# Performance work log

Hardware: AMD Instinct MI355X
Metric: run time of the kernel (lower is better)

Reference implementation:

```python
import jax, jax.numpy as jnp
import numpy as np

EPS = 1e-5

def _bn(h, g, b, m, v):
    # inference-mode batchnorm, channel axis = 1
    shape = (1, -1) + (1,) * (h.ndim - 2)
    scale = g.reshape(shape) / jnp.sqrt(v.reshape(shape) + EPS)
    return (h - m.reshape(shape)) * scale + b.reshape(shape)

def setup_inputs() -> dict:
    B, Cin, Cout, N, K = 2, 64, 64, 50000, 16
    key = jax.random.key(0)
    ks = jax.random.split(key, 24)
    def bn_params(i, C):
        g = 1.0 + 0.1 * jax.random.normal(ks[i], (C,), jnp.float32)
        b = 0.1 * jax.random.normal(ks[i + 1], (C,), jnp.float32)
        m = 0.1 * jax.random.normal(ks[i + 2], (C,), jnp.float32)
        v = jax.random.uniform(ks[i + 3], (C,), jnp.float32, 0.5, 1.5)
        return g, b, m, v
    bn0_g, bn0_b, bn0_m, bn0_v = bn_params(0, Cin)
    bn2a_g, bn2a_b, bn2a_m, bn2a_v = bn_params(4, Cin)
    bn2b_g, bn2b_b, bn2b_m, bn2b_v = bn_params(8, Cout)
    x = jax.random.normal(ks[12], (B, Cin, N), jnp.float32)
    neighbors = jax.random.randint(ks[13], (B, K, N), 0, N, jnp.int32)
    w1 = 0.05 * jax.random.normal(ks[14], (Cout, Cin), jnp.float32)
    b1 = 0.05 * jax.random.normal(ks[15], (Cout,), jnp.float32)
    w2a = 0.05 * jax.random.normal(ks[16], (Cout, Cin), jnp.float32)
    w2b = 0.05 * jax.random.normal(ks[17], (Cout, Cout), jnp.float32)
    wf = 0.05 * jax.random.normal(ks[18], (Cout, 2 * Cout), jnp.float32)
    bf = 0.05 * jax.random.normal(ks[19], (Cout,), jnp.float32)
    return {"x": x, "neighbors": neighbors,
            "bn0_g": bn0_g, "bn0_b": bn0_b, "bn0_m": bn0_m, "bn0_v": bn0_v,
            "w1": w1, "b1": b1,
            "bn2a_g": bn2a_g, "bn2a_b": bn2a_b, "bn2a_m": bn2a_m, "bn2a_v": bn2a_v,
            "w2a": w2a,
            "bn2b_g": bn2b_g, "bn2b_b": bn2b_b, "bn2b_m": bn2b_m, "bn2b_v": bn2b_v,
            "w2b": w2b, "wf": wf, "bf": bf}

def reference(x, neighbors, bn0_g, bn0_b, bn0_m, bn0_v, w1, b1,
              bn2a_g, bn2a_b, bn2a_m, bn2a_v, w2a,
              bn2b_g, bn2b_b, bn2b_m, bn2b_v, w2b, wf, bf):
    # x: (B, Cin, N), neighbors: (B, K, N) int indices into N
    xn = _bn(x, bn0_g, bn0_b, bn0_m, bn0_v)                    # BatchNorm1d
    point = jnp.einsum('oc,bcn->bon', w1, xn) + b1[None, :, None]  # conv1 (1x1)
    idx = neighbors[:, 1:, :]                                   # (B, K-1, N); skip self (col 0)
    # gathered[b,c,k,n] = xn[b,c, idx[b,k,n]]
    gathered = jax.vmap(lambda xb, ib: xb[:, ib])(xn, idx)      # (B, C, K-1, N)
    diff = jnp.transpose(gathered, (0, 1, 3, 2)) - xn[:, :, :, None]  # (B, C, N, K-1)
    h = _bn(diff, bn2a_g, bn2a_b, bn2a_m, bn2a_v)               # BatchNorm2d
    h = jnp.einsum('oc,bcnk->bonk', w2a, h)                     # Conv2d 1x1, no bias
    h = jax.nn.relu(_bn(h, bn2b_g, bn2b_b, bn2b_m, bn2b_v))
    h = jnp.einsum('oc,bcnk->bonk', w2b, h)                     # Conv2d 1x1, no bias
    neigh = h.max(axis=-1)                                      # max over K-1 neighbors
    cat = jnp.concatenate([point, neigh], axis=1)               # (B, 2*Cout, N)
    return jnp.einsum('oc,bcn->bon', wf, cat) + bf[None, :, None]
```

## Files before the change

### kernel.cpp

```cpp
#include <hip/hip_runtime.h>
#include <hip/hip_bf16.h>

typedef __bf16 bf16x8 __attribute__((ext_vector_type(8)));
typedef float f32x4 __attribute__((ext_vector_type(4)));
typedef unsigned int uint32x4 __attribute__((ext_vector_type(4)));

#define NPT 50000

#define OFF_Y    0u
#define OFF_PRM  12800000u
#define OFF_W2   12801024u
#define OFF_WP   12809216u
#define OFF_W2B  12817408u
#define OFF_WN   12825600u
#define OFF_FLAG 12833792u

__global__ __launch_bounds__(256) void precompute_kernel(
    const void* bn0_g, const void* bn0_b, const void* bn0_m, const void* bn0_v,
    const void* w1, const void* b1,
    const void* bn2a_g, const void* bn2a_b, const void* bn2a_m, const void* bn2a_v,
    const void* w2a,
    const void* bn2b_g, const void* bn2b_b, const void* bn2b_m, const void* bn2b_v,
    const void* w2b, const void* wf, const void* bfv,
    float* __restrict__ prm, __bf16* __restrict__ W2bf, __bf16* __restrict__ Wpbf,
    __bf16* __restrict__ W2Bbf, __bf16* __restrict__ Wnbf, int* __restrict__ flagp)
{
    __shared__ __bf16 w1s[4096];
    __shared__ __bf16 wfs[8192];
    __shared__ __bf16 w2as[4096];
    __shared__ float b1s[64], bfs[64], s2a[64], t2a[64], s2b[64], t2b[64];
    __shared__ int sflag;
    int t = threadIdx.x;

    if (t == 0) {
        const unsigned short* u = (const unsigned short*)bn0_v;
        int cnt = 0;
        for (int i = 0; i < 64; ++i) {
            float f = __uint_as_float(((unsigned int)u[i]) << 16);
            if (f > 0.4f && f < 1.6f) cnt++;
        }
        int fv = (cnt >= 60) ? 1 : 0;
        sflag = fv;
        *flagp = fv;
    }
    __syncthreads();
    int fl = sflag;

    if (fl) {
        const __bf16* W1  = (const __bf16*)w1;
        const __bf16* W2A = (const __bf16*)w2a;
        const __bf16* WF  = (const __bf16*)wf;
        const __bf16* W2B = (const __bf16*)w2b;
        for (int i = t; i < 4096; i += 256) { w1s[i] = W1[i]; w2as[i] = W2A[i]; W2Bbf[i] = W2B[i]; }
        for (int i = t; i < 8192; i += 256) wfs[i] = WF[i];
        if (t < 64) {
            float s0 = (float)((const __bf16*)bn0_g)[t] / sqrtf((float)((const __bf16*)bn0_v)[t] + 1e-5f);
            prm[t] = s0;
            prm[64 + t] = (float)((const __bf16*)bn0_b)[t] - (float)((const __bf16*)bn0_m)[t] * s0;
            float sa = (float)((const __bf16*)bn2a_g)[t] / sqrtf((float)((const __bf16*)bn2a_v)[t] + 1e-5f);
            s2a[t] = sa;
            t2a[t] = (float)((const __bf16*)bn2a_b)[t] - (float)((const __bf16*)bn2a_m)[t] * sa;
            float sb = (float)((const __bf16*)bn2b_g)[t] / sqrtf((float)((const __bf16*)bn2b_v)[t] + 1e-5f);
            s2b[t] = sb;
            t2b[t] = (float)((const __bf16*)bn2b_b)[t] - (float)((const __bf16*)bn2b_m)[t] * sb;
            b1s[t] = (float)((const __bf16*)b1)[t];
            bfs[t] = (float)((const __bf16*)bfv)[t];
        }
    } else {
        const float* W1  = (const float*)w1;
        const float* W2A = (const float*)w2a;
        const float* WF  = (const float*)wf;
        const float* W2B = (const float*)w2b;
        for (int i = t; i < 4096; i += 256) { w1s[i] = (__bf16)W1[i]; w2as[i] = (__bf16)W2A[i]; W2Bbf[i] = (__bf16)W2B[i]; }
        for (int i = t; i < 8192; i += 256) wfs[i] = (__bf16)WF[i];
        if (t < 64) {
            float s0 = ((const float*)bn0_g)[t] / sqrtf(((const float*)bn0_v)[t] + 1e-5f);
            prm[t] = s0;
            prm[64 + t] = ((const float*)bn0_b)[t] - ((const float*)bn0_m)[t] * s0;
            float sa = ((const float*)bn2a_g)[t] / sqrtf(((const float*)bn2a_v)[t] + 1e-5f);
            s2a[t] = sa;
            t2a[t] = ((const float*)bn2a_b)[t] - ((const float*)bn2a_m)[t] * sa;
            float sb = ((const float*)bn2b_g)[t] / sqrtf(((const float*)bn2b_v)[t] + 1e-5f);
            s2b[t] = sb;
            t2b[t] = ((const float*)bn2b_b)[t] - ((const float*)bn2b_m)[t] * sb;
            b1s[t] = ((const float*)b1)[t];
            bfs[t] = ((const float*)bfv)[t];
        }
    }
    __syncthreads();

    for (int e = t; e < 4096; e += 256) {
        int o = e >> 6, c = e & 63;
        W2bf[e] = (__bf16)((float)w2as[e] * s2a[c] * s2b[o]);
        Wnbf[e] = wfs[o * 128 + 64 + c];
        float acc = 0.f;
        for (int m = 0; m < 64; ++m)
            acc += (float)wfs[o * 128 + m] * (float)w1s[m * 64 + c];
        Wpbf[e] = (__bf16)acc;
    }
    if (t < 64) {
        float acc = 0.f, accb = 0.f;
        for (int c = 0; c < 64; ++c) {
            acc  += (float)w2as[t * 64 + c] * t2a[c];
            accb += (float)wfs[t * 128 + c] * b1s[c];
        }
        prm[128 + t] = s2b[t] * acc + t2b[t];
        prm[192 + t] = accb + bfs[t];
    }
}

__global__ __launch_bounds__(256) void pass1_kernel(
    const void* x, const float* __restrict__ prm,
    const __bf16* __restrict__ W2bf, __bf16* __restrict__ Y,
    const int* __restrict__ flagp)
{
    __shared__ float xs[64][65];
    int bid = blockIdx.x;
    int b = bid / 782;
    int n0 = (bid % 782) * 64;
    int npts = NPT - n0; if (npts > 64) npts = 64;
    int fl = *flagp;

    if (npts == 64) {
        if (fl) {
            const __bf16* xb = (const __bf16*)x + (size_t)b * 64 * NPT + n0;
            for (int i = threadIdx.x; i < 512; i += 256) {
                int c = i >> 3, q = (i & 7) * 8;
                bf16x8 v = *(const bf16x8*)(xb + (size_t)c * NPT + q);
                #pragma unroll
                for (int e = 0; e < 8; ++e)
                    xs[q + e][c] = fmaf((float)v[e], prm[c], prm[64 + c]);
            }
        } else {
            const float* xb = (const float*)x + (size_t)b * 64 * NPT + n0;
            for (int i = threadIdx.x; i < 1024; i += 256) {
                int c = i >> 4, q = (i & 15) * 4;
                float4 v = *(const float4*)(xb + (size_t)c * NPT + q);
                xs[q + 0][c] = fmaf(v.x, prm[c], prm[64 + c]);
                xs[q + 1][c] = fmaf(v.y, prm[c], prm[64 + c]);
                xs[q + 2][c] = fmaf(v.z, prm[c], prm[64 + c]);
                xs[q + 3][c] = fmaf(v.w, prm[c], prm[64 + c]);
            }
        }
    } else {
        if (fl) {
            const __bf16* xb = (const __bf16*)x + (size_t)b * 64 * NPT;
            for (int i = threadIdx.x; i < 4096; i += 256) {
                int c = i >> 6, p = i & 63;
                float v = (p < npts) ? (float)xb[(size_t)c * NPT + n0 + p] : 0.f;
                xs[p][c] = fmaf(v, prm[c], prm[64 + c]);
            }
        } else {
            const float* xb = (const float*)x + (size_t)b * 64 * NPT;
            for (int i = threadIdx.x; i < 4096; i += 256) {
                int c = i >> 6, p = i & 63;
                float v = (p < npts) ? xb[(size_t)c * NPT + n0 + p] : 0.f;
                xs[p][c] = fmaf(v, prm[c], prm[64 + c]);
            }
        }
    }
    __syncthreads();

    int wid = threadIdx.x >> 6, lane = threadIdx.x & 63;
    int pl = (wid << 4) + (lane & 15);
    int hq = lane >> 4;
    int c0 = hq << 3;

    bf16x8 a0, a1;
    #pragma unroll
    for (int i = 0; i < 8; ++i) {
        a0[i] = (__bf16)xs[pl][c0 + i];
        a1[i] = (__bf16)xs[pl][c0 + 32 + i];
    }

    int ob = lane & 15;
    f32x4 accY[4];
    #pragma unroll
    for (int nt = 0; nt < 4; ++nt) {
        bf16x8 w20 = *(const bf16x8*)(W2bf + (ob + 16 * nt) * 64 + c0);
        bf16x8 w21 = *(const bf16x8*)(W2bf + (ob + 16 * nt) * 64 + c0 + 32);
        f32x4 z = {0.f, 0.f, 0.f, 0.f};
        accY[nt] = __builtin_amdgcn_mfma_f32_16x16x32_bf16(a0, w20, z, 0, 0, 0);
        accY[nt] = __builtin_amdgcn_mfma_f32_16x16x32_bf16(a1, w21, accY[nt], 0, 0, 0);
    }

    #pragma unroll
    for (int nt = 0; nt < 4; ++nt) {
        #pragma unroll
        for (int i = 0; i < 4; ++i) {
            int prow = (wid << 4) + (hq << 2) + i;
            if (prow < npts)
                Y[((size_t)b * NPT + n0 + prow) * 64 + ob + 16 * nt] = (__bf16)accY[nt][i];
        }
    }
}

__global__ __launch_bounds__(256, 2) void pass2_kernel(
    const int* __restrict__ nbr, const __bf16* __restrict__ Y,
    const void* x, const float* __restrict__ prm,
    const __bf16* __restrict__ W2Bbf, const __bf16* __restrict__ Wnbf,
    const __bf16* __restrict__ Wpbf, void* out, const int* __restrict__ flagp)
{
    __shared__ float ns[2][2][16][69];
    int wid = threadIdx.x >> 6, lane = threadIdx.x & 63;
    int tile = wid >> 1, h = wid & 1;
    int gtile = blockIdx.x * 2 + tile;
    int b = gtile / 3125;
    int n0 = (gtile % 3125) << 4;
    int fl = *flagp;

    int mo = lane & 15;
    int hq = lane >> 4;
    int c0 = hq << 3;
    int nglob = n0 + mo;

    const int* nb_base = nbr + (size_t)b * 16 * NPT + NPT + nglob;
    int kbase = h * 7;
    unsigned int ju[8];
    #pragma unroll
    for (int kk = 0; kk < 8; ++kk) {
        unsigned long long a = (unsigned long long)(nb_base + (size_t)(kbase + kk) * NPT);
        asm volatile("global_load_dword %0, %1, off" : "=v"(ju[kk]) : "v"(a) : "memory");
    }
    unsigned int xr[16];
    if (fl) {
        const __bf16* xp = (const __bf16*)x + (size_t)b * 64 * NPT + nglob;
        #pragma unroll
        for (int i = 0; i < 16; ++i) {
            int c = c0 + (i >> 3) * 32 + (i & 7);
            unsigned long long a = (unsigned long long)(xp + (size_t)c * NPT);
            asm volatile("global_load_ushort %0, %1, off" : "=v"(xr[i]) : "v"(a) : "memory");
        }
    } else {
        const float* xp = (const float*)x + (size_t)b * 64 * NPT + nglob;
        #pragma unroll
        for (int i = 0; i < 16; ++i) {
            int c = c0 + (i >> 3) * 32 + (i & 7);
            unsigned long long a = (unsigned long long)(xp + (size_t)c * NPT);
            asm volatile("global_load_dword %0, %1, off" : "=v"(xr[i]) : "v"(a) : "memory");
        }
    }

    const __bf16* yrow = Y + ((size_t)b * NPT + nglob) * 64;
    bf16x8 yn0 = *(const bf16x8*)(yrow + c0);
    bf16x8 yn1 = *(const bf16x8*)(yrow + c0 + 32);
    bf16x8 wA[4][2];
    #pragma unroll
    for (int mt = 0; mt < 4; ++mt) {
        wA[mt][0] = *(const bf16x8*)(W2Bbf + (mo + 16 * mt) * 64 + c0);
        wA[mt][1] = *(const bf16x8*)(W2Bbf + (mo + 16 * mt) * 64 + c0 + 32);
    }

    asm volatile("s_waitcnt vmcnt(0)" ::: "memory");
    __builtin_amdgcn_sched_barrier(0);

    uint32x4 g0[8], g1[8];
    const char* ybase = (const char*)Y + (size_t)b * NPT * 128 + hq * 16;
    #pragma unroll
    for (int kk = 0; kk < 8; ++kk) {
        unsigned long long a0 = (unsigned long long)(ybase + (size_t)ju[kk] * 128);
        asm volatile("global_load_dwordx4 %0, %1, off" : "=v"(g0[kk]) : "v"(a0) : "memory");
        asm volatile("global_load_dwordx4 %0, %1, off offset:64" : "=v"(g1[kk]) : "v"(a0) : "memory");
    }

    float mv0[8], mv1[8];
    #pragma unroll
    for (int i = 0; i < 8; ++i) {
        mv0[i] = prm[128 + c0 + i]      - (float)yn0[i];
        mv1[i] = prm[128 + c0 + 32 + i] - (float)yn1[i];
    }

    f32x4 vmax[4];
    #pragma unroll
    for (int mt = 0; mt < 4; ++mt) vmax[mt] = {-3.0e38f, -3.0e38f, -3.0e38f, -3.0e38f};

    asm volatile("s_waitcnt vmcnt(0)" ::: "memory");
    __builtin_amdgcn_sched_barrier(0);

    #pragma unroll
    for (int kk = 0; kk < 8; ++kk) {
        bf16x8 y0 = __builtin_bit_cast(bf16x8, g0[kk]);
        bf16x8 y1 = __builtin_bit_cast(bf16x8, g1[kk]);
        bf16x8 t0, t1;
        #pragma unroll
        for (int i = 0; i < 8; ++i) {
            t0[i] = (__bf16)fmaxf((float)y0[i] + mv0[i], 0.f);
            t1[i] = (__bf16)fmaxf((float)y1[i] + mv1[i], 0.f);
        }
        #pragma unroll
        for (int mt = 0; mt < 4; ++mt) {
            f32x4 hh = {0.f, 0.f, 0.f, 0.f};
            hh = __builtin_amdgcn_mfma_f32_16x16x32_bf16(wA[mt][0], t0, hh, 0, 0, 0);
            hh = __builtin_amdgcn_mfma_f32_16x16x32_bf16(wA[mt][1], t1, hh, 0, 0, 0);
            #pragma unroll
            for (int i = 0; i < 4; ++i) vmax[mt][i] = fmaxf(vmax[mt][i], hh[i]);
        }
    }

    #pragma unroll
    for (int mt = 0; mt < 4; ++mt)
        #pragma unroll
        for (int i = 0; i < 4; ++i)
            ns[tile][h][mo][16 * mt + (hq << 2) + i] = vmax[mt][i];

    __syncthreads();

    bf16x8 nb2[2];
    #pragma unroll
    for (int ks = 0; ks < 2; ++ks)
        #pragma unroll
        for (int i = 0; i < 8; ++i) {
            int c = c0 + 32 * ks + i;
            nb2[ks][i] = (__bf16)fmaxf(ns[tile][0][mo][c], ns[tile][1][mo][c]);
        }

    bf16x8 xnb[2];
    #pragma unroll
    for (int i = 0; i < 16; ++i) {
        int c = c0 + (i >> 3) * 32 + (i & 7);
        float v = fl ? __uint_as_float(xr[i] << 16) : __uint_as_float(xr[i]);
        xnb[i >> 3][i & 7] = (__bf16)fmaf(v, prm[c], prm[64 + c]);
    }

    #pragma unroll
    for (int q = 0; q < 2; ++q) {
        int mt = 2 * h + q;
        bf16x8 wn0 = *(const bf16x8*)(Wnbf + (mo + 16 * mt) * 64 + c0);
        bf16x8 wn1 = *(const bf16x8*)(Wnbf + (mo + 16 * mt) * 64 + c0 + 32);
        bf16x8 wp0 = *(const bf16x8*)(Wpbf + (mo + 16 * mt) * 64 + c0);
        bf16x8 wp1 = *(const bf16x8*)(Wpbf + (mo + 16 * mt) * 64 + c0 + 32);
        f32x4 acc = *(const f32x4*)(prm + 192 + 16 * mt + 4 * hq);
        acc = __builtin_amdgcn_mfma_f32_16x16x32_bf16(wp0, xnb[0], acc, 0, 0, 0);
        acc = __builtin_amdgcn_mfma_f32_16x16x32_bf16(wp1, xnb[1], acc, 0, 0, 0);
        acc = __builtin_amdgcn_mfma_f32_16x16x32_bf16(wn0, nb2[0], acc, 0, 0, 0);
        acc = __builtin_amdgcn_mfma_f32_16x16x32_bf16(wn1, nb2[1], acc, 0, 0, 0);

        if (fl) {
            __bf16* ob = (__bf16*)out + (size_t)b * 64 * NPT + nglob;
            #pragma unroll
            for (int i = 0; i < 4; ++i)
                ob[(size_t)(16 * mt + (hq << 2) + i) * NPT] = (__bf16)acc[i];
        } else {
            float* ob = (float*)out + (size_t)b * 64 * NPT + nglob;
            #pragma unroll
            for (int i = 0; i < 4; ++i)
                ob[(size_t)(16 * mt + (hq << 2) + i) * NPT] = acc[i];
        }
    }
}

extern "C" void kernel_launch(void* const* d_in, const int* in_sizes, int n_in,
                              void* d_out, int out_size, void* d_ws, size_t ws_size,
                              hipStream_t stream) {
    const void* x      = d_in[0];
    const int*  nbr    = (const int*)d_in[1];

    char* ws = (char*)d_ws;
    __bf16* Y     = (__bf16*)(ws + OFF_Y);
    float*  prm   = (float*)(ws + OFF_PRM);
    __bf16* W2bf  = (__bf16*)(ws + OFF_W2);
    __bf16* Wpbf  = (__bf16*)(ws + OFF_WP);
    __bf16* W2Bbf = (__bf16*)(ws + OFF_W2B);
    __bf16* Wnbf  = (__bf16*)(ws + OFF_WN);
    int*    flagp = (int*)(ws + OFF_FLAG);

    precompute_kernel<<<1, 256, 0, stream>>>(
        d_in[2], d_in[3], d_in[4], d_in[5], d_in[6], d_in[7],
        d_in[8], d_in[9], d_in[10], d_in[11], d_in[12],
        d_in[13], d_in[14], d_in[15], d_in[16], d_in[17], d_in[18], d_in[19],
        prm, W2bf, Wpbf, W2Bbf, Wnbf, flagp);

    pass1_kernel<<<1564, 256, 0, stream>>>(x, prm, W2bf, Y, flagp);

    pass2_kernel<<<3125, 256, 0, stream>>>(nbr, Y, x, prm, W2Bbf, Wnbf, Wpbf, d_out, flagp);
}
```

Baseline: 203.6 us.

## Split pass2 neighbor work across four waves and parallelize the Wp precompute

The pass2 kernel now assigns one 16-point tile per block, with four waves each handling four neighbors instead of two waves handling eight. Partial maxima are combined through shared memory, and only two waves then load x and run the final projection. Launch bounds rise to four blocks per SM, aiming for more in-flight gathers and lower register pressure. The folded wf·w1 product is also spread over 16 extra precompute blocks instead of being computed serially in one block. The trade-offs are that half the waves sit idle during the epilogue and the x loads no longer overlap with the gathers.

```diff
diff --git a/kernel.cpp b/kernel.cpp
--- a/kernel.cpp
+++ b/kernel.cpp
@@ -14,6 +14,16 @@
 #define OFF_W2B  12817408u
 #define OFF_WN   12825600u
 #define OFF_FLAG 12833792u
+
+__device__ __forceinline__ int detect_bf16(const void* bn0_v) {
+    const unsigned short* u = (const unsigned short*)bn0_v;
+    int cnt = 0;
+    for (int i = 0; i < 64; ++i) {
+        float f = __uint_as_float(((unsigned int)u[i]) << 16);
+        if (f > 0.4f && f < 1.6f) cnt++;
+    }
+    return (cnt >= 60) ? 1 : 0;
+}
 
 __global__ __launch_bounds__(256) void precompute_kernel(
     const void* bn0_g, const void* bn0_b, const void* bn0_m, const void* bn0_v,
@@ -25,33 +35,53 @@
     float* __restrict__ prm, __bf16* __restrict__ W2bf, __bf16* __restrict__ Wpbf,
     __bf16* __restrict__ W2Bbf, __bf16* __restrict__ Wnbf, int* __restrict__ flagp)
 {
-    __shared__ __bf16 w1s[4096];
+    __shared__ int sflag;
+    int t = threadIdx.x;
+    if (t == 0) sflag = detect_bf16(bn0_v);
+    __syncthreads();
+    int fl = sflag;
+
+    if (blockIdx.x < 16) {
+        __shared__ __bf16 w1s[4096];
+        __shared__ float wfr[4][64];
+        int ob = blockIdx.x * 4;
+        if (fl) {
+            const __bf16* W1 = (const __bf16*)w1;
+            const __bf16* WF = (const __bf16*)wf;
+            for (int i = t; i < 4096; i += 256) w1s[i] = W1[i];
+            if (t < 256) {
+                int o = t >> 6, m = t & 63;
+                wfr[o][m] = (float)WF[(ob + o) * 128 + m];
+            }
+        } else {
+            const float* W1 = (const float*)w1;
+            const float* WF = (const float*)wf;
+            for (int i = t; i < 4096; i += 256) w1s[i] = (__bf16)W1[i];
+            if (t < 256) {
+                int o = t >> 6, m = t & 63;
+                wfr[o][m] = WF[(ob + o) * 128 + m];
+            }
+        }
+        __syncthreads();
+        int o = t >> 6, c = t & 63;
+        float acc = 0.f;
+        for (int m = 0; m < 64; ++m)
+            acc += wfr[o][m] * (float)w1s[m * 64 + c];
+        Wpbf[(ob + o) * 64 + c] = (__bf16)acc;
+        return;
+    }
+
     __shared__ __bf16 wfs[8192];
     __shared__ __bf16 w2as[4096];
     __shared__ float b1s[64], bfs[64], s2a[64], t2a[64], s2b[64], t2b[64];
-    __shared__ int sflag;
-    int t = threadIdx.x;
-
-    if (t == 0) {
-        const unsigned short* u = (const unsigned short*)bn0_v;
-        int cnt = 0;
-        for (int i = 0; i < 64; ++i) {
-            float f = __uint_as_float(((unsigned int)u[i]) << 16);
-            if (f > 0.4f && f < 1.6f) cnt++;
-        }
-        int fv = (cnt >= 60) ? 1 : 0;
-        sflag = fv;
-        *flagp = fv;
-    }
-    __syncthreads();
-    int fl = sflag;
+
+    if (t == 0) *flagp = fl;
 
     if (fl) {
-        const __bf16* W1  = (const __bf16*)w1;
         const __bf16* W2A = (const __bf16*)w2a;
         const __bf16* WF  = (const __bf16*)wf;
         const __bf16* W2B = (const __bf16*)w2b;
-        for (int i = t; i < 4096; i += 256) { w1s[i] = W1[i]; w2as[i] = W2A[i]; W2Bbf[i] = W2B[i]; }
+        for (int i = t; i < 4096; i += 256) { w2as[i] = W2A[i]; W2Bbf[i] = W2B[i]; }
         for (int i = t; i < 8192; i += 256) wfs[i] = WF[i];
         if (t < 64) {
             float s0 = (float)((const __bf16*)bn0_g)[t] / sqrtf((float)((const __bf16*)bn0_v)[t] + 1e-5f);
@@ -67,11 +97,10 @@
             bfs[t] = (float)((const __bf16*)bfv)[t];
         }
     } else {
-        const float* W1  = (const float*)w1;
         const float* W2A = (const float*)w2a;
         const float* WF  = (const float*)wf;
         const float* W2B = (const float*)w2b;
-        for (int i = t; i < 4096; i += 256) { w1s[i] = (__bf16)W1[i]; w2as[i] = (__bf16)W2A[i]; W2Bbf[i] = (__bf16)W2B[i]; }
+        for (int i = t; i < 4096; i += 256) { w2as[i] = (__bf16)W2A[i]; W2Bbf[i] = (__bf16)W2B[i]; }
         for (int i = t; i < 8192; i += 256) wfs[i] = (__bf16)WF[i];
         if (t < 64) {
             float s0 = ((const float*)bn0_g)[t] / sqrtf(((const float*)bn0_v)[t] + 1e-5f);
@@ -93,10 +122,6 @@
         int o = e >> 6, c = e & 63;
         W2bf[e] = (__bf16)((float)w2as[e] * s2a[c] * s2b[o]);
         Wnbf[e] = wfs[o * 128 + 64 + c];
-        float acc = 0.f;
-        for (int m = 0; m < 64; ++m)
-            acc += (float)wfs[o * 128 + m] * (float)w1s[m * 64 + c];
-        Wpbf[e] = (__bf16)acc;
     }
     if (t < 64) {
         float acc = 0.f, accb = 0.f;
@@ -195,16 +220,15 @@
     }
 }
 
-__global__ __launch_bounds__(256, 2) void pass2_kernel(
+__global__ __launch_bounds__(256, 4) void pass2_kernel(
     const int* __restrict__ nbr, const __bf16* __restrict__ Y,
     const void* x, const float* __restrict__ prm,
     const __bf16* __restrict__ W2Bbf, const __bf16* __restrict__ Wnbf,
     const __bf16* __restrict__ Wpbf, void* out, const int* __restrict__ flagp)
 {
-    __shared__ float ns[2][2][16][69];
-    int wid = threadIdx.x >> 6, lane = threadIdx.x & 63;
-    int tile = wid >> 1, h = wid & 1;
-    int gtile = blockIdx.x * 2 + tile;
+    __shared__ float ns[4][16][69];
+    int h = threadIdx.x >> 6, lane = threadIdx.x & 63;
+    int gtile = blockIdx.x;
     int b = gtile / 3125;
     int n0 = (gtile % 3125) << 4;
     int fl = *flagp;
@@ -214,31 +238,13 @@
     int c0 = hq << 3;
     int nglob = n0 + mo;
 
-    const int* nb_base = nbr + (size_t)b * 16 * NPT + NPT + nglob;
-    int kbase = h * 7;
-    unsigned int ju[8];
-    #pragma unroll
-    for (int kk = 0; kk < 8; ++kk) {
-        unsigned long long a = (unsigned long long)(nb_base + (size_t)(kbase + kk) * NPT);
+    const int* nb_base = nbr + (size_t)b * 16 * NPT + nglob;
+    unsigned int ju[4];
+    #pragma unroll
+    for (int kk = 0; kk < 4; ++kk) {
+        int kv = 4 * h + kk + 1; if (kv > 15) kv = 15;
+        unsigned long long a = (unsigned long long)(nb_base + (size_t)kv * NPT);
         asm volatile("global_load_dword %0, %1, off" : "=v"(ju[kk]) : "v"(a) : "memory");
-    }
-    unsigned int xr[16];
-    if (fl) {
-        const __bf16* xp = (const __bf16*)x + (size_t)b * 64 * NPT + nglob;
-        #pragma unroll
-        for (int i = 0; i < 16; ++i) {
-            int c = c0 + (i >> 3) * 32 + (i & 7);
-            unsigned long long a = (unsigned long long)(xp + (size_t)c * NPT);
-            asm volatile("global_load_ushort %0, %1, off" : "=v"(xr[i]) : "v"(a) : "memory");
-        }
-    } else {
-        const float* xp = (const float*)x + (size_t)b * 64 * NPT + nglob;
-        #pragma unroll
-        for (int i = 0; i < 16; ++i) {
-            int c = c0 + (i >> 3) * 32 + (i & 7);
-            unsigned long long a = (unsigned long long)(xp + (size_t)c * NPT);
-            asm volatile("global_load_dword %0, %1, off" : "=v"(xr[i]) : "v"(a) : "memory");
-        }
     }
 
     const __bf16* yrow = Y + ((size_t)b * NPT + nglob) * 64;
@@ -254,10 +260,10 @@
     asm volatile("s_waitcnt vmcnt(0)" ::: "memory");
     __builtin_amdgcn_sched_barrier(0);
 
-    uint32x4 g0[8], g1[8];
+    uint32x4 g0[4], g1[4];
     const char* ybase = (const char*)Y + (size_t)b * NPT * 128 + hq * 16;
     #pragma unroll
-    for (int kk = 0; kk < 8; ++kk) {
+    for (int kk = 0; kk < 4; ++kk) {
         unsigned long long a0 = (unsigned long long)(ybase + (size_t)ju[kk] * 128);
         asm volatile("global_load_dwordx4 %0, %1, off" : "=v"(g0[kk]) : "v"(a0) : "memory");
         asm volatile("global_load_dwordx4 %0, %1, off offset:64" : "=v"(g1[kk]) : "v"(a0) : "memory");
@@ -278,7 +284,7 @@
     __builtin_amdgcn_sched_barrier(0);
 
     #pragma unroll
-    for (int kk = 0; kk < 8; ++kk) {
+    for (int kk = 0; kk < 4; ++kk) {
         bf16x8 y0 = __builtin_bit_cast(bf16x8, g0[kk]);
         bf16x8 y1 = __builtin_bit_cast(bf16x8, g1[kk]);
         bf16x8 t0, t1;
@@ -301,50 +307,69 @@
     for (int mt = 0; mt < 4; ++mt)
         #pragma unroll
         for (int i = 0; i < 4; ++i)
-            ns[tile][h][mo][16 * mt + (hq << 2) + i] = vmax[mt][i];
+            ns[h][mo][16 * mt + (hq << 2) + i] = vmax[mt][i];
 
     __syncthreads();
 
-    bf16x8 nb2[2];
-    #pragma unroll
-    for (int ks = 0; ks < 2; ++ks)
-        #pragma unroll
-        for (int i = 0; i < 8; ++i) {
-            int c = c0 + 32 * ks + i;
-            nb2[ks][i] = (__bf16)fmaxf(ns[tile][0][mo][c], ns[tile][1][mo][c]);
-        }
-
-    bf16x8 xnb[2];
-    #pragma unroll
-    for (int i = 0; i < 16; ++i) {
-        int c = c0 + (i >> 3) * 32 + (i & 7);
-        float v = fl ? __uint_as_float(xr[i] << 16) : __uint_as_float(xr[i]);
-        xnb[i >> 3][i & 7] = (__bf16)fmaf(v, prm[c], prm[64 + c]);
-    }
-
-    #pragma unroll
-    for (int q = 0; q < 2; ++q) {
-        int mt = 2 * h + q;
-        bf16x8 wn0 = *(const bf16x8*)(Wnbf + (mo + 16 * mt) * 64 + c0);
-        bf16x8 wn1 = *(const bf16x8*)(Wnbf + (mo + 16 * mt) * 64 + c0 + 32);
-        bf16x8 wp0 = *(const bf16x8*)(Wpbf + (mo + 16 * mt) * 64 + c0);
-        bf16x8 wp1 = *(const bf16x8*)(Wpbf + (mo + 16 * mt) * 64 + c0 + 32);
-        f32x4 acc = *(const f32x4*)(prm + 192 + 16 * mt + 4 * hq);
-        acc = __builtin_amdgcn_mfma_f32_16x16x32_bf16(wp0, xnb[0], acc, 0, 0, 0);
-        acc = __builtin_amdgcn_mfma_f32_16x16x32_bf16(wp1, xnb[1], acc, 0, 0, 0);
-        acc = __builtin_amdgcn_mfma_f32_16x16x32_bf16(wn0, nb2[0], acc, 0, 0, 0);
-        acc = __builtin_amdgcn_mfma_f32_16x16x32_bf16(wn1, nb2[1], acc, 0, 0, 0);
-
+    if (h < 2) {
+        bf16x8 nb2[2];
+        #pragma unroll
+        for (int ks = 0; ks < 2; ++ks)
+            #pragma unroll
+            for (int i = 0; i < 8; ++i) {
+                int c = c0 + 32 * ks + i;
+                float m01 = fmaxf(ns[0][mo][c], ns[1][mo][c]);
+                float m23 = fmaxf(ns[2][mo][c], ns[3][mo][c]);
+                nb2[ks][i] = (__bf16)fmaxf(m01, m23);
+            }
+
+        bf16x8 xnb[2];
         if (fl) {
-            __bf16* ob = (__bf16*)out + (size_t)b * 64 * NPT + nglob;
+            const __bf16* xp = (const __bf16*)x + (size_t)b * 64 * NPT + nglob;
             #pragma unroll
-            for (int i = 0; i < 4; ++i)
-                ob[(size_t)(16 * mt + (hq << 2) + i) * NPT] = (__bf16)acc[i];
+            for (int ks = 0; ks < 2; ++ks)
+                #pragma unroll
+                for (int i = 0; i < 8; ++i) {
+                    int c = c0 + 32 * ks + i;
+                    float v = (float)xp[(size_t)c * NPT];
+                    xnb[ks][i] = (__bf16)fmaf(v, prm[c], prm[64 + c]);
+                }
         } else {
-            float* ob = (float*)out + (size_t)b * 64 * NPT + nglob;
+            const float* xp = (const float*)x + (size_t)b * 64 * NPT + nglob;
             #pragma unroll
-            for (int i = 0; i < 4; ++i)
-                ob[(size_t)(16 * mt + (hq << 2) + i) * NPT] = acc[i];
+            for (int ks = 0; ks < 2; ++ks)
+                #pragma unroll
+                for (int i = 0; i < 8; ++i) {
+                    int c = c0 + 32 * ks + i;
+                    float v = xp[(size_t)c * NPT];
+                    xnb[ks][i] = (__bf16)fmaf(v, prm[c], prm[64 + c]);
+                }
+        }
+
+        #pragma unroll
+        for (int q = 0; q < 2; ++q) {
+            int mt = 2 * h + q;
+            bf16x8 wn0 = *(const bf16x8*)(Wnbf + (mo + 16 * mt) * 64 + c0);
+            bf16x8 wn1 = *(const bf16x8*)(Wnbf + (mo + 16 * mt) * 64 + c0 + 32);
+            bf16x8 wp0 = *(const bf16x8*)(Wpbf + (mo + 16 * mt) * 64 + c0);
+            bf16x8 wp1 = *(const bf16x8*)(Wpbf + (mo + 16 * mt) * 64 + c0 + 32);
+            f32x4 acc = *(const f32x4*)(prm + 192 + 16 * mt + 4 * hq);
+            acc = __builtin_amdgcn_mfma_f32_16x16x32_bf16(wp0, xnb[0], acc, 0, 0, 0);
+            acc = __builtin_amdgcn_mfma_f32_16x16x32_bf16(wp1, xnb[1], acc, 0, 0, 0);
+            acc = __builtin_amdgcn_mfma_f32_16x16x32_bf16(wn0, nb2[0], acc, 0, 0, 0);
+            acc = __builtin_amdgcn_mfma_f32_16x16x32_bf16(wn1, nb2[1], acc, 0, 0, 0);
+
+            if (fl) {
+                __bf16* ob = (__bf16*)out + (size_t)b * 64 * NPT + nglob;
+                #pragma unroll
+                for (int i = 0; i < 4; ++i)
+                    ob[(size_t)(16 * mt + (hq << 2) + i) * NPT] = (__bf16)acc[i];
+            } else {
+                float* ob = (float*)out + (size_t)b * 64 * NPT + nglob;
+                #pragma unroll
+                for (int i = 0; i < 4; ++i)
+                    ob[(size_t)(16 * mt + (hq << 2) + i) * NPT] = acc[i];
+            }
         }
     }
 }
@@ -364,7 +389,7 @@
     __bf16* Wnbf  = (__bf16*)(ws + OFF_WN);
     int*    flagp = (int*)(ws + OFF_FLAG);
 
-    precompute_kernel<<<1, 256, 0, stream>>>(
+    precompute_kernel<<<17, 256, 0, stream>>>(
         d_in[2], d_in[3], d_in[4], d_in[5], d_in[6], d_in[7],
         d_in[8], d_in[9], d_in[10], d_in[11], d_in[12],
         d_in[13], d_in[14], d_in[15], d_in[16], d_in[17], d_in[18], d_in[19],
@@ -372,5 +397,5 @@
 
     pass1_kernel<<<1564, 256, 0, stream>>>(x, prm, W2bf, Y, flagp);
 
-    pass2_kernel<<<3125, 256, 0, stream>>>(nbr, Y, x, prm, W2Bbf, Wnbf, Wpbf, d_out, flagp);
+    pass2_kernel<<<6250, 256, 0, stream>>>(nbr, Y, x, prm, W2Bbf, Wnbf, Wpbf, d_out, flagp);
 }
```

After: 211.9 us. +4.1%, slower.
